# Kernel tuning notes

Measured on AMD Instinct MI355X. Metric: run time of the kernel, lower is better.

The kernel has to match this reference:

```python
import jax, jax.numpy as jnp
import numpy as np

N = 50_000      # nodes
E = 500_000     # directed edges
EMB = 500       # emb_dim (fixed by module)
OUT = 119       # decoder out_dim (num atom types)
L = 5           # encoder num_layer
BN_EPS = 1e-5


def setup_inputs() -> dict:
    key = jax.random.key(0)
    ks = jax.random.split(key, 20)
    d = {}
    # int graph inputs
    atom_type = jax.random.randint(ks[0], (N,), 0, 119)
    chirality = jax.random.randint(ks[1], (N,), 0, 3)
    d["x"] = jnp.stack([atom_type, chirality], axis=1)
    d["edge_index"] = jax.random.randint(ks[2], (2, E), 0, N)
    bond_type = jax.random.randint(ks[3], (E,), 0, 4)  # real bonds (4 = self-loop token)
    bond_dir = jax.random.randint(ks[4], (E,), 0, 3)
    d["edge_attr"] = jnp.stack([bond_type, bond_dir], axis=1)
    d["masked_atom_mask"] = jax.random.bernoulli(ks[5], 0.25, (N,))
    # float params
    f = lambda k, s: (jax.random.normal(k, s) * 0.02).astype(jnp.float32)
    d["atom_emb1"] = f(ks[6], (120, EMB))
    d["atom_emb2"] = f(ks[7], (3, EMB))
    d["enc_eemb1"] = f(ks[8], (L, 6, EMB))
    d["enc_eemb2"] = f(ks[9], (L, 3, EMB))
    d["enc_W1"] = f(ks[10], (L, EMB, 2 * EMB))
    d["enc_b1"] = jnp.zeros((L, 2 * EMB), jnp.float32)
    d["enc_W2"] = f(ks[11], (L, 2 * EMB, EMB))
    d["enc_b2"] = jnp.zeros((L, EMB), jnp.float32)
    d["bn_gamma"] = jnp.ones((L, EMB), jnp.float32)
    d["bn_beta"] = jnp.zeros((L, EMB), jnp.float32)
    d["bn_mean"] = jnp.zeros((L, EMB), jnp.float32)
    d["bn_var"] = jnp.ones((L, EMB), jnp.float32)
    d["prelu_a"] = jnp.float32(0.25)
    d["n2d_W"] = f(ks[12], (EMB, EMB))  # Linear(500,500,bias=False)
    d["dec_eemb1"] = f(ks[13], (6, EMB))
    d["dec_eemb2"] = f(ks[14], (3, EMB))
    d["dec_W1"] = f(ks[15], (EMB, 2 * EMB))
    d["dec_b1"] = jnp.zeros((2 * EMB,), jnp.float32)
    d["dec_W2"] = f(ks[16], (2 * EMB, OUT))
    d["dec_b2"] = jnp.zeros((OUT,), jnp.float32)
    return d


def _gin(h, src, dst, eemb, W1, b1, W2, b2):
    # message = x_j + edge_emb ; aggr='add' ; update = MLP
    msg = h[src] + eemb                                   # [E+N, EMB]
    agg = jax.ops.segment_sum(msg, dst, num_segments=h.shape[0])
    return jax.nn.relu(agg @ W1 + b1) @ W2 + b2


def _forward(x, edge_index, edge_attr, masked_atom_mask,
             atom_emb1, atom_emb2, enc_eemb1, enc_eemb2, enc_W1, enc_b1,
             enc_W2, enc_b2, bn_gamma, bn_beta, bn_mean, bn_var,
             prelu_a, n2d_W, dec_eemb1, dec_eemb2, dec_W1, dec_b1, dec_W2, dec_b2):
    n = x.shape[0]
    loops = jnp.arange(n)
    src = jnp.concatenate([edge_index[0], loops])         # add self loops
    dst = jnp.concatenate([edge_index[1], loops])
    ea0 = jnp.concatenate([edge_attr[:, 0], jnp.full((n,), 4, edge_attr.dtype)])
    ea1 = jnp.concatenate([edge_attr[:, 1], jnp.zeros((n,), edge_attr.dtype)])

    # GNN encoder
    h = atom_emb1[x[:, 0]] + atom_emb2[x[:, 1]]           # [N, EMB]
    for l in range(L):
        eemb = enc_eemb1[l][ea0] + enc_eemb2[l][ea1]
        h = _gin(h, src, dst, eemb, enc_W1[l], enc_b1[l], enc_W2[l], enc_b2[l])
        # BatchNorm1d in eval mode (running stats)
        h = (h - bn_mean[l]) * jax.lax.rsqrt(bn_var[l] + BN_EPS) * bn_gamma[l] + bn_beta[l]
        if l < L - 1:
            h = jax.nn.relu(h)
        # drop_ratio=0 -> no dropout

    # encoder_to_decoder: PReLU -> Linear(bias=False)
    h = jnp.where(h >= 0, h, prelu_a * h) @ n2d_W
    # zero out masked atoms
    h = jnp.where(masked_atom_mask[:, None], jnp.float32(0), h)

    # GINConv decoder -> [N, 119]
    eemb = dec_eemb1[ea0] + dec_eemb2[ea1]
    return _gin(h, src, dst, eemb, dec_W1, dec_b1, dec_W2, dec_b2)


def reference(x, edge_index, edge_attr, masked_atom_mask,
              atom_emb1, atom_emb2, enc_eemb1, enc_eemb2, enc_W1, enc_b1,
              enc_W2, enc_b2, bn_gamma, bn_beta, bn_mean, bn_var,
              prelu_a, n2d_W, dec_eemb1, dec_eemb2, dec_W1, dec_b1, dec_W2, dec_b2):
    return _forward(x, edge_index, edge_attr, masked_atom_mask,
                    atom_emb1, atom_emb2, enc_eemb1, enc_eemb2, enc_W1, enc_b1,
                    enc_W2, enc_b2, bn_gamma, bn_beta, bn_mean, bn_var,
                    prelu_a, n2d_W, dec_eemb1, dec_eemb2, dec_W1, dec_b1,
                    dec_W2, dec_b2)
```

## Files before the change

kernel.cpp:

```cpp
#include <hip/hip_runtime.h>
#include <stdint.h>

typedef unsigned short u16;
typedef __bf16 bf16x8 __attribute__((ext_vector_type(8)));
typedef float f32x4 __attribute__((ext_vector_type(4)));

enum { EPI_TMP = 0, EPI_BN = 1, EPI_N2D = 2, EPI_OUT = 3, EPI_BNPRELU = 4 };

__device__ __forceinline__ u16 f2bf(float x) {
  unsigned int u = __float_as_uint(x);
  u += 0x7FFFu + ((u >> 16) & 1u);
  return (u16)(u >> 16);
}
__device__ __forceinline__ float bf2f(u16 b) {
  return __uint_as_float(((unsigned int)b) << 16);
}
__device__ __forceinline__ float bflo(unsigned int u) { return __uint_as_float(u << 16); }
__device__ __forceinline__ float bfhi(unsigned int u) { return __uint_as_float(u & 0xFFFF0000u); }
__device__ __forceinline__ ushort4 pack4(float a, float b, float c, float d) {
  return make_ushort4(f2bf(a), f2bf(b), f2bf(c), f2bf(d));
}

struct F4 { float x, y, z, w; };
__device__ __forceinline__ F4 ld4(const float* p) {
  float4 v = *(const float4*)p;
  return {v.x, v.y, v.z, v.w};
}

typedef const void __attribute__((address_space(1))) as1cv;
typedef void __attribute__((address_space(3))) as3v;
__device__ __forceinline__ void gld16(const void* g, void* l) {
  __builtin_amdgcn_global_load_lds((as1cv*)g, (as3v*)l, 16, 0, 0);
}


__global__ void k_detect(const unsigned int* __restrict__ m, int nwords, int* __restrict__ flag) {
  int viol = 0;
  for (int i = blockIdx.x * blockDim.x + threadIdx.x; i < nwords; i += gridDim.x * blockDim.x) {
    unsigned int u = m[i];
    if (u > 1u) viol |= 1;
    if (u != 0u && u != 0x3F800000u) viol |= 2;
  }
  if (viol) atomicOr(flag, viol);
}

__global__ void k_norm(const void* __restrict__ raw, const int* __restrict__ flag,
                       unsigned char* __restrict__ mout, int N) {
  int f = *flag;
  for (int v = blockIdx.x * blockDim.x + threadIdx.x; v < N; v += gridDim.x * blockDim.x) {
    unsigned char b;
    if ((f & 1) == 0)       b = (unsigned char)(((const int*)raw)[v] != 0);
    else if ((f & 2) == 0)  b = (unsigned char)(((const float*)raw)[v] != 0.0f);
    else                    b = (unsigned char)(((const unsigned char*)raw)[v] != 0);
    mout[v] = b;
  }
}

__global__ void k_count(const int* __restrict__ ei, int E, int* __restrict__ deg) {
  for (int e = blockIdx.x * blockDim.x + threadIdx.x; e < E; e += gridDim.x * blockDim.x)
    atomicAdd(&deg[ei[E + e]], 1);
}

__global__ __launch_bounds__(1024)
void k_scanA(const int* __restrict__ deg, int* __restrict__ out,
             int* __restrict__ bsum, int n) {
  __shared__ int lws[17];
  const int tid = threadIdx.x, lane = tid & 63, wv = tid >> 6;
  const int i = blockIdx.x * 1024 + tid;
  const int v = (i < n) ? deg[i] : 0;
  int x = v;
#pragma unroll
  for (int d = 1; d < 64; d <<= 1) {
    int y = __shfl_up(x, d, 64);
    if (lane >= d) x += y;
  }
  if (lane == 63) lws[wv] = x;
  __syncthreads();
  if (tid == 0) {
    int run = 0;
#pragma unroll
    for (int k = 0; k < 16; ++k) { int t = lws[k]; lws[k] = run; run += t; }
    lws[16] = run;
  }
  __syncthreads();
  if (i < n) out[i] = x - v + lws[wv];
  if (tid == 0) bsum[blockIdx.x] = lws[16];
}

__global__ void k_scanB(int* __restrict__ bsum, int* __restrict__ offN, int nc) {
  const int t = threadIdx.x;
  const int v = (t < nc) ? bsum[t] : 0;
  int x = v;
#pragma unroll
  for (int d = 1; d < 64; d <<= 1) {
    int y = __shfl_up(x, d, 64);
    if (t >= d) x += y;
  }
  if (t < nc) bsum[t] = x - v;
  if (t == nc - 1) *offN = x;
}

__global__ void k_scanC(int* __restrict__ off_, const int* __restrict__ bsum, int n) {
  int i = blockIdx.x * blockDim.x + threadIdx.x;
  if (i < n) off_[i] += bsum[i >> 10];
}

__global__ void k_fill(const int* __restrict__ ei, const int* __restrict__ ea, int E,
                       int* __restrict__ cur, int* __restrict__ elist) {
  for (int e = blockIdx.x * blockDim.x + threadIdx.x; e < E; e += gridDim.x * blockDim.x) {
    int s = ei[e];
    int d = ei[E + e];
    int a0 = ea[2 * e], a1 = ea[2 * e + 1];
    int pos = atomicAdd(&cur[d], 1);
    elist[pos] = s | (a0 << 20) | (a1 << 23);
  }
}

__global__ void k_counts(const int* __restrict__ off_, const int* __restrict__ elist,
                         unsigned char* __restrict__ cnts, int N) {
  int v = blockIdx.x * blockDim.x + threadIdx.x;
  if (v >= N) return;
  int c0=0,c1=0,c2=0,c3=0,c4=0,c5=0,d0=0,d1=0,d2=0;
  const int e1 = off_[v + 1];
  for (int e = off_[v]; e < e1; ++e) {
    int p = elist[e];
    int a = (p >> 20) & 7, b = (p >> 23) & 3;
    c0 += (a==0); c1 += (a==1); c2 += (a==2);
    c3 += (a==3); c4 += (a==4); c5 += (a==5);
    d0 += (b==0); d1 += (b==1); d2 += (b==2);
  }
  unsigned char* cp = cnts + v * 12;
  cp[0]=(unsigned char)c0; cp[1]=(unsigned char)c1; cp[2]=(unsigned char)c2;
  cp[3]=(unsigned char)c3; cp[4]=(unsigned char)c4; cp[5]=(unsigned char)c5;
  cp[6]=(unsigned char)d0; cp[7]=(unsigned char)d1; cp[8]=(unsigned char)d2;
}

__global__ void k_tab(const float* __restrict__ ee1, const float* __restrict__ ee2,
                      const float* __restrict__ de1, const float* __restrict__ de2,
                      float* __restrict__ tab) {
  int idx = blockIdx.x * blockDim.x + threadIdx.x;
  if (idx >= 54 * 512) return;
  int col = idx & 511, row = (idx >> 9) % 9, l = idx / (9 * 512);
  float v = 0.f;
  if (col < 500) {
    if (l < 5) v = (row < 6) ? ee1[((size_t)l * 6 + row) * 500 + col]
                             : ee2[((size_t)l * 3 + (row - 6)) * 500 + col];
    else       v = (row < 6) ? de1[(size_t)row * 500 + col]
                             : de2[(size_t)(row - 6) * 500 + col];
  }
  tab[idx] = v;
}

__global__ void k_conv_w(const float* __restrict__ src, u16* __restrict__ dst,
                         int K, int Nsrc, int Kpad, int Npad, int L) {
  size_t total = (size_t)L * Npad * Kpad;
  for (size_t idx = blockIdx.x * (size_t)blockDim.x + threadIdx.x; idx < total;
       idx += (size_t)gridDim.x * blockDim.x) {
    int k = (int)(idx % (size_t)Kpad);
    size_t r = idx / (size_t)Kpad;
    int n = (int)(r % (size_t)Npad);
    int l = (int)(r / (size_t)Npad);
    float v = 0.0f;
    if (k < K && n < Nsrc) v = src[((size_t)l * K + k) * Nsrc + n];
    dst[idx] = f2bf(v);
  }
}

__global__ void k_init_h(const int* __restrict__ x, const float* __restrict__ e1,
                         const float* __restrict__ e2, u16* __restrict__ h, int nReal) {
  int total = nReal * 128;
  for (int i = blockIdx.x * blockDim.x + threadIdx.x; i < total; i += gridDim.x * blockDim.x) {
    int v = i >> 7, q = i & 127, j = q << 2;
    u16* hp = h + ((size_t)v << 9) + j;
    if (j < 500) {
      int a = x[2 * v], c = x[2 * v + 1];
      F4 va = ld4(e1 + (size_t)a * 500 + j);
      F4 vc = ld4(e2 + (size_t)c * 500 + j);
      *(ushort4*)hp = pack4(va.x + vc.x, va.y + vc.y, va.z + vc.z, va.w + vc.w);
    } else {
      *(ushort4*)hp = make_ushort4(0, 0, 0, 0);
    }
  }
}

__device__ __forceinline__ void add8(float* s, uint4 u) {
  s[0] += bflo(u.x); s[1] += bfhi(u.x);
  s[2] += bflo(u.y); s[3] += bfhi(u.y);
  s[4] += bflo(u.z); s[5] += bfhi(u.z);
  s[6] += bflo(u.w); s[7] += bfhi(u.w);
}

__global__ __launch_bounds__(256, 6)
void k_aggregate(const u16* __restrict__ h, const int* __restrict__ off_,
                 const int* __restrict__ elist, const unsigned char* __restrict__ cnts,
                 const float* __restrict__ tab, u16* __restrict__ agg, int nReal) {
  const int lane = threadIdx.x & 63, wv = threadIdx.x >> 6;
  const int v = (blockIdx.x << 2) | wv;
  if (v >= nReal) return;
  const int j = lane << 3;
  float s[8];
  {
    uint4 u = *(const uint4*)(h + ((size_t)v << 9) + j);
    s[0] = bflo(u.x); s[1] = bfhi(u.x); s[2] = bflo(u.y); s[3] = bfhi(u.y);
    s[4] = bflo(u.z); s[5] = bfhi(u.z); s[6] = bflo(u.w); s[7] = bfhi(u.w);
  }
  const int eE = off_[v + 1];
  int e = off_[v];
  for (; e + 8 <= eE; e += 8) {
    const int p0 = elist[e]     & 0xFFFFF, p1 = elist[e + 1] & 0xFFFFF;
    const int p2 = elist[e + 2] & 0xFFFFF, p3 = elist[e + 3] & 0xFFFFF;
    const int p4 = elist[e + 4] & 0xFFFFF, p5 = elist[e + 5] & 0xFFFFF;
    const int p6 = elist[e + 6] & 0xFFFFF, p7 = elist[e + 7] & 0xFFFFF;
    uint4 u0 = *(const uint4*)(h + ((size_t)p0 << 9) + j);
    uint4 u1 = *(const uint4*)(h + ((size_t)p1 << 9) + j);
    uint4 u2 = *(const uint4*)(h + ((size_t)p2 << 9) + j);
    uint4 u3 = *(const uint4*)(h + ((size_t)p3 << 9) + j);
    uint4 u4 = *(const uint4*)(h + ((size_t)p4 << 9) + j);
    uint4 u5 = *(const uint4*)(h + ((size_t)p5 << 9) + j);
    uint4 u6 = *(const uint4*)(h + ((size_t)p6 << 9) + j);
    uint4 u7 = *(const uint4*)(h + ((size_t)p7 << 9) + j);
    add8(s, u0); add8(s, u1); add8(s, u2); add8(s, u3);
    add8(s, u4); add8(s, u5); add8(s, u6); add8(s, u7);
  }
  for (; e + 4 <= eE; e += 4) {
    uint4 u0 = *(const uint4*)(h + ((size_t)(elist[e]     & 0xFFFFF) << 9) + j);
    uint4 u1 = *(const uint4*)(h + ((size_t)(elist[e + 1] & 0xFFFFF) << 9) + j);
    uint4 u2 = *(const uint4*)(h + ((size_t)(elist[e + 2] & 0xFFFFF) << 9) + j);
    uint4 u3 = *(const uint4*)(h + ((size_t)(elist[e + 3] & 0xFFFFF) << 9) + j);
    add8(s, u0); add8(s, u1); add8(s, u2); add8(s, u3);
  }
  for (; e < eE; ++e) {
    uint4 u = *(const uint4*)(h + ((size_t)(elist[e] & 0xFFFFF) << 9) + j);
    add8(s, u);
  }
  const unsigned char* cp = cnts + v * 12;
  constexpr float ex[9] = {0.f,0.f,0.f,0.f,1.f,0.f, 1.f,0.f,0.f};
#pragma unroll
  for (int k = 0; k < 9; ++k) {
    const float ck = (float)cp[k] + ex[k];
    F4 t0 = ld4(tab + (k << 9) + j);
    F4 t1 = ld4(tab + (k << 9) + j + 4);
    s[0] += ck * t0.x; s[1] += ck * t0.y; s[2] += ck * t0.z; s[3] += ck * t0.w;
    s[4] += ck * t1.x; s[5] += ck * t1.y; s[6] += ck * t1.z; s[7] += ck * t1.w;
  }
  auto pk = [](float a, float b) {
    return (unsigned int)f2bf(a) | ((unsigned int)f2bf(b) << 16);
  };
  uint4 o = {pk(s[0], s[1]), pk(s[2], s[3]), pk(s[4], s[5]), pk(s[6], s[7])};
  *(uint4*)(agg + ((size_t)v << 9) + j) = o;
}

struct EpiParams {
  const float* bias;
  const float* mean; const float* var; const float* gamma; const float* beta;
  const unsigned char* mask;
  const float* pa;
  float* outF;
  u16* outH;
  int ldOut, nReal, mReal, relu;
};

#define EPI_STRIDE 136

template<int EPI>
__global__ __launch_bounds__(256, 3)
void k_gemm(const u16* __restrict__ A, const u16* __restrict__ B,
            int ldA, int Kpad, int Ntiles, int NWG, EpiParams P) {
  __shared__ __align__(16) u16 smem[128 * EPI_STRIDE];

  const int tid = threadIdx.x;
  const int w = tid >> 6, lane = tid & 63;
  const int q = NWG >> 3, r = NWG & 7;
  const int xcd = blockIdx.x & 7, ii = blockIdx.x >> 3;
  const int wg = (xcd < r ? xcd * (q + 1) : r * (q + 1) + (xcd - r) * q) + ii;
  const int mt = wg / Ntiles, nt = wg % Ntiles;
  const int wm = w >> 1, wn = w & 1;

  f32x4 acc[4][4] = {};
  const size_t arow = (size_t)mt * 128, brow = (size_t)nt * 128;
  const int Ksteps = Kpad >> 6;

  for (int ks = 0; ks < Ksteps; ++ks) {
    const int kb = ks << 6;
#pragma unroll
    for (int it = 0; it < 4; ++it) {
      const int idx = (it << 8) | tid;
      const int row = idx >> 3, s = idx & 7;
      const int col = kb + ((s ^ (row & 7)) << 3);
      u16* dst = smem + (((it << 8) | (w << 6)) << 3);
      gld16(A + (arow + row) * (size_t)ldA + col, dst);
      gld16(B + (brow + row) * (size_t)Kpad + col, dst + 8192);
    }
    asm volatile("s_waitcnt vmcnt(0)" ::: "memory");
    __syncthreads();

#pragma unroll
    for (int kk = 0; kk < 2; ++kk) {
      const int ko8 = (kk << 2) | (lane >> 4);
      const int sw = (ko8 ^ (lane & 7)) << 3;
      bf16x8 af[4], bfr[4];
#pragma unroll
      for (int m = 0; m < 4; ++m)
        af[m] = *(const bf16x8*)(smem + ((((wm << 6) | (m << 4) | (lane & 15))) << 6) + sw);
#pragma unroll
      for (int n = 0; n < 4; ++n)
        bfr[n] = *(const bf16x8*)(smem + 8192 + ((((wn << 6) | (n << 4) | (lane & 15))) << 6) + sw);
#pragma unroll
      for (int m = 0; m < 4; ++m)
#pragma unroll
        for (int n = 0; n < 4; ++n)
          acc[m][n] = __builtin_amdgcn_mfma_f32_16x16x32_bf16(af[m], bfr[n], acc[m][n], 0, 0, 0);
    }
    __syncthreads();
  }

  const int rb0 = mt * 128, cb0 = nt * 128;
  const int rloc = (wm << 6) | ((lane >> 4) << 2);
  const int cloc = (wn << 6) | (lane & 15);

  if constexpr (EPI != EPI_OUT) {
    float alpha = 0.f;
    if constexpr (EPI == EPI_BNPRELU) alpha = *P.pa;
#pragma unroll
    for (int n = 0; n < 4; ++n) {
      const int col = cloc + (n << 4);
      const int colg = cb0 + col;
      const bool cok = colg < P.nReal;
      float bias = 0.f, bnS = 0.f, bnB = 0.f;
      if constexpr (EPI == EPI_TMP) {
        if (cok) bias = P.bias[colg];
      }
      if constexpr (EPI == EPI_BN || EPI == EPI_BNPRELU) {
        if (cok) {
          bias = P.bias[colg];
          bnS = rsqrtf(P.var[colg] + 1e-5f) * P.gamma[colg];
          bnB = P.beta[colg] - P.mean[colg] * bnS;
        }
      }
#pragma unroll
      for (int m = 0; m < 4; ++m) {
#pragma unroll
        for (int rr = 0; rr < 4; ++rr) {
          const int row = rloc + (m << 4) + rr;
          float z = acc[m][n][rr];
          if constexpr (EPI == EPI_TMP) {
            z = fmaxf(z + bias, 0.f);
          } else if constexpr (EPI == EPI_BN) {
            z = (z + bias) * bnS + bnB;
            if (P.relu) z = fmaxf(z, 0.f);
          } else if constexpr (EPI == EPI_BNPRELU) {
            z = (z + bias) * bnS + bnB;
            z = z >= 0.f ? z : alpha * z;
          } else {
            const int rowg = rb0 + row;
            if (rowg < P.mReal && P.mask[rowg]) z = 0.f;
          }
          smem[row * EPI_STRIDE + col] = f2bf(z);
        }
      }
    }
    __syncthreads();
#pragma unroll
    for (int it = 0; it < 8; ++it) {
      const int idx = (it << 8) | tid;
      const int row = idx >> 4, c8 = idx & 15;
      uint4 vv = *(const uint4*)(smem + row * EPI_STRIDE + (c8 << 3));
      *(uint4*)(P.outH + (size_t)(rb0 + row) * P.ldOut + cb0 + (c8 << 3)) = vv;
    }
  } else {
    float* sf = (float*)smem;
#pragma unroll
    for (int p = 0; p < 2; ++p) {
      __syncthreads();
      if (wm == p) {
#pragma unroll
        for (int n = 0; n < 4; ++n) {
          const int col = cloc + (n << 4);
          const float bias = (cb0 + col < P.nReal) ? P.bias[cb0 + col] : 0.f;
#pragma unroll
          for (int m = 0; m < 4; ++m)
#pragma unroll
            for (int rr = 0; rr < 4; ++rr) {
              const int lrow = ((lane >> 4) << 2) + (m << 4) + rr;
              sf[lrow * 132 + col] = acc[m][n][rr] + bias;
            }
        }
      }
      __syncthreads();
      const size_t flat0 = (size_t)(rb0 + (p << 6)) * 119;
      const size_t flatEnd = (size_t)P.mReal * 119;
#pragma unroll 2
      for (int it = 0; it < 30; ++it) {
        const int fidx = it * 256 + tid;
        if (fidx < 64 * 119) {
          const int row = fidx / 119;
          const int col = fidx - row * 119;
          const size_t g = flat0 + fidx;
          if (g < flatEnd) P.outF[g] = sf[row * 132 + col];
        }
      }
    }
  }
}

__global__ void k_fail(float* out, int n, float val) {
  for (int i = blockIdx.x * blockDim.x + threadIdx.x; i < n; i += gridDim.x * blockDim.x)
    out[i] = (i == 0) ? val : 0.f;
}

static inline size_t alup(size_t x) { return (x + 255) & ~(size_t)255; }

extern "C" void kernel_launch(void* const* d_in, const int* in_sizes, int n_in,
                              void* d_out, int out_size, void* d_ws, size_t ws_size,
                              hipStream_t stream) {
  (void)n_in;
  const int N = in_sizes[0] / 2;
  const int E = in_sizes[1] / 2;
  const int Mpad = (N + 127) / 128 * 128;
  const int MT = Mpad / 128;

  size_t off = 0;
  auto plan = [&](size_t b) -> size_t { size_t p = off; off += alup(b); return p; };
  const size_t o_h    = plan((size_t)Mpad * 512 * 2);
  const size_t o_agg  = plan((size_t)Mpad * 512 * 2);
  const size_t o_tmp  = plan((size_t)Mpad * 1024 * 2);
  const size_t o_w1   = plan(5ull * 1024 * 512 * 2);
  const size_t o_w2   = plan(5ull * 512 * 1024 * 2);
  const size_t o_nd   = plan(512ull * 512 * 2);
  const size_t o_d1   = plan(1024ull * 512 * 2);
  const size_t o_d2   = plan(128ull * 1024 * 2);
  const size_t o_tab  = plan(54ull * 512 * 4);
  const size_t o_offv = plan((size_t)(N + 1) * 4);
  const size_t o_cur  = plan((size_t)N * 4);
  const size_t o_el   = plan((size_t)E * 4);
  const size_t o_mask = plan((size_t)N);
  const size_t o_cnt  = plan((size_t)N * 12);
  const size_t o_bsum = plan(1024);
  const size_t o_flag = plan(256);
  const size_t need = off;

  if (ws_size < need) {
    k_fail<<<1024, 256, 0, stream>>>((float*)d_out, out_size, -(float)(ws_size >> 20));
    return;
  }

  char* ws = (char*)d_ws;
  u16* h     = (u16*)(ws + o_h);
  u16* agg   = (u16*)(ws + o_agg);
  u16* tmp   = (u16*)(ws + o_tmp);
  u16* w1H   = (u16*)(ws + o_w1);
  u16* w2H   = (u16*)(ws + o_w2);
  u16* ndH   = (u16*)(ws + o_nd);
  u16* d1H   = (u16*)(ws + o_d1);
  u16* d2H   = (u16*)(ws + o_d2);
  float* tab = (float*)(ws + o_tab);
  int* offv  = (int*)(ws + o_offv);
  int* cur   = (int*)(ws + o_cur);
  int* elist = (int*)(ws + o_el);
  unsigned char* mask = (unsigned char*)(ws + o_mask);
  unsigned char* cnts = (unsigned char*)(ws + o_cnt);
  int* bsum  = (int*)(ws + o_bsum);
  int* flag  = (int*)(ws + o_flag);

  const int* x   = (const int*)d_in[0];
  const int* ei  = (const int*)d_in[1];
  const int* ea  = (const int*)d_in[2];
  const void* mraw = d_in[3];
  const float* ae1 = (const float*)d_in[4];
  const float* ae2 = (const float*)d_in[5];
  const float* ee1 = (const float*)d_in[6];
  const float* ee2 = (const float*)d_in[7];
  const float* W1  = (const float*)d_in[8];
  const float* b1  = (const float*)d_in[9];
  const float* W2  = (const float*)d_in[10];
  const float* b2  = (const float*)d_in[11];
  const float* gamma = (const float*)d_in[12];
  const float* beta  = (const float*)d_in[13];
  const float* mean  = (const float*)d_in[14];
  const float* var   = (const float*)d_in[15];
  const float* pa    = (const float*)d_in[16];
  const float* n2dW  = (const float*)d_in[17];
  const float* de1   = (const float*)d_in[18];
  const float* de2   = (const float*)d_in[19];
  const float* dW1   = (const float*)d_in[20];
  const float* db1   = (const float*)d_in[21];
  const float* dW2   = (const float*)d_in[22];
  const float* db2   = (const float*)d_in[23];

  hipMemsetAsync(flag, 0, 4, stream);
  hipMemsetAsync(cur, 0, (size_t)N * 4, stream);
  k_detect<<<256, 256, 0, stream>>>((const unsigned int*)mraw, N / 4, flag);
  k_norm<<<(N + 255) / 256, 256, 0, stream>>>(mraw, flag, mask, N);
  k_count<<<2048, 256, 0, stream>>>(ei, E, cur);
  const int nchunks = (N + 1023) / 1024;
  k_scanA<<<nchunks, 1024, 0, stream>>>(cur, offv, bsum, N);
  k_scanB<<<1, 64, 0, stream>>>(bsum, offv + N, nchunks);
  k_scanC<<<(N + 255) / 256, 256, 0, stream>>>(offv, bsum, N);
  hipMemcpyAsync(cur, offv, (size_t)N * 4, hipMemcpyDeviceToDevice, stream);
  k_fill<<<2048, 256, 0, stream>>>(ei, ea, E, cur, elist);
  k_counts<<<(N + 255) / 256, 256, 0, stream>>>(offv, elist, cnts, N);
  k_tab<<<(54 * 512 + 255) / 256, 256, 0, stream>>>(ee1, ee2, de1, de2, tab);

  k_conv_w<<<2048, 256, 0, stream>>>(W1, w1H, 500, 1000, 512, 1024, 5);
  k_conv_w<<<2048, 256, 0, stream>>>(W2, w2H, 1000, 500, 1024, 512, 5);
  k_conv_w<<<1024, 256, 0, stream>>>(n2dW, ndH, 500, 500, 512, 512, 1);
  k_conv_w<<<1024, 256, 0, stream>>>(dW1, d1H, 500, 1000, 512, 1024, 1);
  k_conv_w<<<1024, 256, 0, stream>>>(dW2, d2H, 1000, 119, 1024, 128, 1);
  k_init_h<<<4096, 256, 0, stream>>>(x, ae1, ae2, h, N);

  const int aggGrid = (N + 3) / 4;
  EpiParams P{};

  for (int l = 0; l < 5; ++l) {
    k_aggregate<<<aggGrid, 256, 0, stream>>>(h, offv, elist, cnts,
                                             tab + (size_t)l * 9 * 512, agg, N);
    P = EpiParams{};
    P.bias = b1 + (size_t)l * 1000;
    P.outH = tmp; P.ldOut = 1024; P.nReal = 1000; P.mReal = Mpad; P.relu = 1;
    k_gemm<EPI_TMP><<<MT * 8, 256, 0, stream>>>(
        agg, w1H + (size_t)l * 1024 * 512, 512, 512, 8, MT * 8, P);

    P = EpiParams{};
    P.bias = b2 + (size_t)l * 500;
    P.mean = mean + (size_t)l * 500; P.var = var + (size_t)l * 500;
    P.gamma = gamma + (size_t)l * 500; P.beta = beta + (size_t)l * 500;
    if (l < 4) {
      P.outH = h; P.ldOut = 512; P.nReal = 500; P.mReal = Mpad; P.relu = 1;
      k_gemm<EPI_BN><<<MT * 4, 256, 0, stream>>>(
          tmp, w2H + (size_t)l * 512 * 1024, 1024, 1024, 4, MT * 4, P);
    } else {
      P.pa = pa;
      P.outH = agg; P.ldOut = 512; P.nReal = 500; P.mReal = Mpad; P.relu = 0;
      k_gemm<EPI_BNPRELU><<<MT * 4, 256, 0, stream>>>(
          tmp, w2H + (size_t)l * 512 * 1024, 1024, 1024, 4, MT * 4, P);
    }
  }

  P = EpiParams{};
  P.outH = h; P.mask = mask; P.ldOut = 512; P.nReal = 500; P.mReal = N;
  k_gemm<EPI_N2D><<<MT * 4, 256, 0, stream>>>(agg, ndH, 512, 512, 4, MT * 4, P);

  k_aggregate<<<aggGrid, 256, 0, stream>>>(h, offv, elist, cnts,
                                           tab + (size_t)5 * 9 * 512, agg, N);
  P = EpiParams{};
  P.bias = db1; P.outH = tmp; P.ldOut = 1024; P.nReal = 1000; P.mReal = Mpad; P.relu = 1;
  k_gemm<EPI_TMP><<<MT * 8, 256, 0, stream>>>(agg, d1H, 512, 512, 8, MT * 8, P);

  P = EpiParams{};
  P.bias = db2; P.outF = (float*)d_out; P.ldOut = 119; P.nReal = 119; P.mReal = N;
  k_gemm<EPI_OUT><<<MT * 1, 256, 0, stream>>>(tmp, d2H, 1024, 1024, 1, MT, P);
}
```

Measured before the change: 1.365 ms.

## Double-buffer GEMM LDS tiles with K-step 32 and prefetch next tile

```diff
diff --git a/kernel.cpp b/kernel.cpp
--- a/kernel.cpp
+++ b/kernel.cpp
@@ -262,6 +262,8 @@
 
 #define EPI_STRIDE 136
 
+__device__ __forceinline__ int xr4(int r) { return ((r & 3) ^ ((r >> 2) & 3)); }
+
 template<int EPI>
 __global__ __launch_bounds__(256, 3)
 void k_gemm(const u16* __restrict__ A, const u16* __restrict__ B,
@@ -278,40 +280,46 @@
 
   f32x4 acc[4][4] = {};
   const size_t arow = (size_t)mt * 128, brow = (size_t)nt * 128;
-  const int Ksteps = Kpad >> 6;
-
-  for (int ks = 0; ks < Ksteps; ++ks) {
-    const int kb = ks << 6;
-#pragma unroll
-    for (int it = 0; it < 4; ++it) {
-      const int idx = (it << 8) | tid;
-      const int row = idx >> 3, s = idx & 7;
-      const int col = kb + ((s ^ (row & 7)) << 3);
-      u16* dst = smem + (((it << 8) | (w << 6)) << 3);
-      gld16(A + (arow + row) * (size_t)ldA + col, dst);
-      gld16(B + (brow + row) * (size_t)Kpad + col, dst + 8192);
-    }
-    asm volatile("s_waitcnt vmcnt(0)" ::: "memory");
+  const int Tn = Kpad >> 5;
+  const int fr = lane & 15, fq = lane >> 4;
+
+  auto stage = [&](int d, int t) {
+    const int kb = t << 5;
+#pragma unroll
+    for (int it = 0; it < 2; ++it) {
+      const int row = (it << 6) + (tid >> 2);
+      const int s = tid & 3;
+      const int col = kb + ((s ^ xr4(row)) << 3);
+      const int dstu = (d << 13) + (((it << 8) + tid) << 3);
+      gld16(A + (arow + row) * (size_t)ldA + col, smem + dstu);
+      gld16(B + (brow + row) * (size_t)Kpad + col, smem + dstu + 4096);
+    }
+  };
+
+  stage(0, 0);
+  __syncthreads();
+
+  int cur = 0;
+  for (int t = 0; t < Tn; ++t) {
+    if (t + 1 < Tn) stage(cur ^ 1, t + 1);
+    bf16x8 af[4], bfr[4];
+#pragma unroll
+    for (int m = 0; m < 4; ++m) {
+      const int rr = (wm << 6) | (m << 4) | fr;
+      af[m] = *(const bf16x8*)(smem + (cur << 13) + rr * 32 + ((fq ^ xr4(rr)) << 3));
+    }
+#pragma unroll
+    for (int n = 0; n < 4; ++n) {
+      const int rr = (wn << 6) | (n << 4) | fr;
+      bfr[n] = *(const bf16x8*)(smem + (cur << 13) + 4096 + rr * 32 + ((fq ^ xr4(rr)) << 3));
+    }
+#pragma unroll
+    for (int m = 0; m < 4; ++m)
+#pragma unroll
+      for (int n = 0; n < 4; ++n)
+        acc[m][n] = __builtin_amdgcn_mfma_f32_16x16x32_bf16(af[m], bfr[n], acc[m][n], 0, 0, 0);
     __syncthreads();
-
-#pragma unroll
-    for (int kk = 0; kk < 2; ++kk) {
-      const int ko8 = (kk << 2) | (lane >> 4);
-      const int sw = (ko8 ^ (lane & 7)) << 3;
-      bf16x8 af[4], bfr[4];
-#pragma unroll
-      for (int m = 0; m < 4; ++m)
-        af[m] = *(const bf16x8*)(smem + ((((wm << 6) | (m << 4) | (lane & 15))) << 6) + sw);
-#pragma unroll
-      for (int n = 0; n < 4; ++n)
-        bfr[n] = *(const bf16x8*)(smem + 8192 + ((((wn << 6) | (n << 4) | (lane & 15))) << 6) + sw);
-#pragma unroll
-      for (int m = 0; m < 4; ++m)
-#pragma unroll
-        for (int n = 0; n < 4; ++n)
-          acc[m][n] = __builtin_amdgcn_mfma_f32_16x16x32_bf16(af[m], bfr[n], acc[m][n], 0, 0, 0);
-    }
-    __syncthreads();
+    cur ^= 1;
   }
 
   const int rb0 = mt * 128, cb0 = nt * 128;
```

Result: slower. 1.450 ms (+6.2%).
